# Kernel tuning notes

Measured on AMD Instinct MI355X. Metric: run time of the kernel, lower is better.

Reference implementation:

```python
import jax, jax.numpy as jnp
import numpy as np

V = [642, 2562, 10242]
NGT = 8000
NSAMP = 4000
CHAM_W = [3000.0, 3000.0, 3000.0]
LAP_C = [0.2, 1.0, 1.0]
CHAM_OPP = 0.55
W_LAP, W_MOVE, W_EDGE, W_NORM = 1500.0, 50.0, 359.0, 0.5


def _normalize(x, axis=-1):
    n = jnp.linalg.norm(x, axis=axis, keepdims=True)
    return x / jnp.maximum(n, 1e-12)


def _mse(a, b):
    return jnp.mean((a - b) ** 2)


def _sample_points(verts, faces, n, key):
    # uniform face pick + uniform barycentric (sqrt trick), matches sample_point_cloud
    kf, kb = jax.random.split(key)
    fidx = jax.random.randint(kf, (n,), 0, faces.shape[0])
    tri = verts[faces[fidx]]  # [n,3,3]
    uv = jax.random.uniform(kb, (n, 2), dtype=verts.dtype)
    r1 = jnp.sqrt(uv[:, 0]); r2 = uv[:, 1]
    w = jnp.stack([1.0 - r1, r1 * (1.0 - r2), r1 * r2], axis=1)  # [n,3]
    return jnp.einsum('nk,nkd->nd', w, tri)


def _chamfer(gt, pred):
    # squared pairwise distances [B,Ng,Np]
    d = (jnp.sum(gt ** 2, -1)[:, :, None] + jnp.sum(pred ** 2, -1)[:, None, :]
         - 2.0 * jnp.einsum('bnd,bmd->bnm', gt, pred))
    dist1 = jnp.min(d, 2); idx1 = jnp.argmin(d, 2)  # gt -> nearest pred
    dist2 = jnp.min(d, 1); idx2 = jnp.argmin(d, 1)  # pred -> nearest gt
    return dist1, dist2, idx1, idx2


def _laplace_coord(x, lap):
    # x [B,n,3], lap [n,10]: 8 neighbor idx (-1 invalid), self idx, count
    idx = lap[:, :8]
    mask = idx < 0
    safe = jnp.where(mask, 0, idx)
    v = x[:, safe]  # [B,n,8,3]
    v = jnp.where(mask[None, :, :, None], 0.0, v)
    cnt = lap[:, -1].astype(x.dtype)
    return x - v.sum(2) / cnt[None, :, None]


def _block(gt, gtn, pred, pred_bef, lap, edges, faces, key, cham_w, lap_c, block_idx):
    samp = _sample_points(pred[0], faces, NSAMP, key)[None]
    sample_pred = jnp.concatenate([pred, samp], 1)
    d1, d2, _i1, i2 = _chamfer(gt, sample_pred)
    chamfer = cham_w * (jnp.mean(d1) + CHAM_OPP * jnp.mean(d2))
    e = _normalize(pred[:, edges[:, 0]] - pred[:, edges[:, 1]], 2)
    nn = jnp.take_along_axis(gtn, i2[..., None], axis=1)  # nearest gt normal per pred pt
    nrm = _normalize(nn[:, edges[:, 0]], 2)
    normal = jnp.mean(jnp.abs(jnp.sum(e * nrm, 2)))
    edge = _mse(pred[:, edges[:, 0]], pred[:, edges[:, 1]]) * 3.0
    lap_l = lap_c * _mse(_laplace_coord(pred_bef, lap), _laplace_coord(pred, lap)) * 3.0
    move = lap_c * _mse(pred_bef, pred) * 3.0 if block_idx > 0 else 0.0
    return chamfer, normal, edge, lap_l, move


def setup_inputs() -> dict:
    key = jax.random.key(0)
    ks = jax.random.split(key, 8)
    inp = {}
    inp['gt_points'] = jax.random.normal(ks[0], (1, NGT, 3), jnp.float32)
    inp['gt_normals'] = _normalize(jax.random.normal(ks[1], (1, NGT, 3), jnp.float32), 2)
    for i, v in enumerate(V):
        kp, kb, ke, kf, kl = jax.random.split(ks[2 + i], 5)
        pc = jax.random.normal(kp, (1, v, 3), jnp.float32)
        inp[f'pred_coord_{i}'] = pc
        inp[f'pred_before_{i}'] = pc + 0.1 * jax.random.normal(kb, (1, v, 3), jnp.float32)
        inp[f'edges_{i}'] = jax.random.randint(ke, (3 * v, 2), 0, v, dtype=jnp.int32)
        inp[f'faces_{i}'] = jax.random.randint(kf, (2 * v, 3), 0, v, dtype=jnp.int32)
        nbr = jax.random.randint(kl, (v, 8), 0, v, dtype=jnp.int32)
        valid = (nbr % 7) != 0
        valid = valid.at[:, 0].set(True)  # count >= 1
        cnt = valid.sum(1).astype(jnp.int32)
        nbr_m = jnp.where(valid, nbr, -1)
        self_idx = jnp.arange(v, dtype=jnp.int32)[:, None]
        inp[f'lap_idx_{i}'] = jnp.concatenate([nbr_m, self_idx, cnt[:, None]], 1)
    return inp


def reference(gt_points, gt_normals,
              pred_coord_0, pred_before_0, edges_0, faces_0, lap_idx_0,
              pred_coord_1, pred_before_1, edges_1, faces_1, lap_idx_1,
              pred_coord_2, pred_before_2, edges_2, faces_2, lap_idx_2):
    skey = jax.random.key(42)
    preds = [pred_coord_0, pred_coord_1, pred_coord_2]
    befs = [pred_before_0, pred_before_1, pred_before_2]
    edges = [edges_0, edges_1, edges_2]
    faces = [faces_0, faces_1, faces_2]
    laps = [lap_idx_0, lap_idx_1, lap_idx_2]
    ch = nl = el = ll = ml = 0.0
    for i in range(3):
        c, n, e, l, m = _block(gt_points, gt_normals, preds[i], befs[i], laps[i],
                               edges[i], faces[i], jax.random.fold_in(skey, i),
                               CHAM_W[i], LAP_C[i], i)
        ch += c; nl += n; el += e; ll += l; ml += m
    loss = ch + W_LAP * ll + W_MOVE * ml + W_EDGE * el + W_NORM * nl
    return loss
```

## Files before the change

kernel.cpp:

```cpp
#include <hip/hip_runtime.h>
#include <stdint.h>

#define NGT 8000
#define NSAMP 4000
#define QT 4
#define QB 1024
#define CH 384

struct Params {
  const float* gt;
  const float* gtn;
  const float* pred[3];
  const float* bef[3];
  const int*   edges[3];
  const int*   faces[3];
  const int*   lap[3];
  float* S[3];
  unsigned int* mb1[3];
  unsigned long long* mb2a[3];
  unsigned int* mb2b[3];
  float* acc;
  unsigned int* counter;
  unsigned int* init_base;
  int init_words;
  int v[3], M[3], E[3], F[3];
  int z1, z2;
};

__device__ __forceinline__ unsigned int ford(float f){
  unsigned int b = __float_as_uint(f);
  return b ^ ((b >> 31) ? 0xFFFFFFFFu : 0x80000000u);
}
__device__ __forceinline__ float funord(unsigned int u){
  unsigned int b = u ^ ((u >> 31) ? 0x80000000u : 0xFFFFFFFFu);
  return __uint_as_float(b);
}

__device__ __forceinline__ uint32_t rotl32(uint32_t x, int d){ return (x<<d)|(x>>(32-d)); }

__device__ __forceinline__ void tf2x32(uint32_t k0, uint32_t k1, uint32_t c0, uint32_t c1,
                                       uint32_t& o0, uint32_t& o1){
  uint32_t ks2 = k0 ^ k1 ^ 0x1BD11BDAu;
  uint32_t x0 = c0 + k0, x1 = c1 + k1;
  x0+=x1; x1=rotl32(x1,13); x1^=x0;
  x0+=x1; x1=rotl32(x1,15); x1^=x0;
  x0+=x1; x1=rotl32(x1,26); x1^=x0;
  x0+=x1; x1=rotl32(x1, 6); x1^=x0;
  x0+=k1; x1+=ks2+1u;
  x0+=x1; x1=rotl32(x1,17); x1^=x0;
  x0+=x1; x1=rotl32(x1,29); x1^=x0;
  x0+=x1; x1=rotl32(x1,16); x1^=x0;
  x0+=x1; x1=rotl32(x1,24); x1^=x0;
  x0+=ks2; x1+=k0+2u;
  x0+=x1; x1=rotl32(x1,13); x1^=x0;
  x0+=x1; x1=rotl32(x1,15); x1^=x0;
  x0+=x1; x1=rotl32(x1,26); x1^=x0;
  x0+=x1; x1=rotl32(x1, 6); x1^=x0;
  x0+=k0; x1+=k1+3u;
  x0+=x1; x1=rotl32(x1,17); x1^=x0;
  x0+=x1; x1=rotl32(x1,29); x1^=x0;
  x0+=x1; x1=rotl32(x1,16); x1^=x0;
  x0+=x1; x1=rotl32(x1,24); x1^=x0;
  x0+=k1; x1+=ks2+4u;
  x0+=x1; x1=rotl32(x1,13); x1^=x0;
  x0+=x1; x1=rotl32(x1,15); x1^=x0;
  x0+=x1; x1=rotl32(x1,26); x1^=x0;
  x0+=x1; x1=rotl32(x1, 6); x1^=x0;
  x0+=ks2; x1+=k0+5u;
  o0=x0; o1=x1;
}

__device__ __forceinline__ uint32_t rbits(uint32_t k0, uint32_t k1, uint32_t idx, uint32_t total){
  uint32_t half = total>>1, o0, o1;
  if (idx < half){ tf2x32(k0,k1, idx, idx+half, o0, o1); return o0; }
  tf2x32(k0,k1, idx-half, idx, o0, o1); return o1;
}

__global__ __launch_bounds__(256) void prep_kernel(Params p){
  if (blockIdx.z == 0){
    if (blockIdx.y != 0) return;
    int wdi = blockIdx.x*256 + threadIdx.x;
    if (wdi < p.init_words)
      p.init_base[wdi] = (wdi < 64) ? 0u : 0xFFFFFFFFu;
    return;
  }
  int i = blockIdx.y;
  int s = blockIdx.x*256 + threadIdx.x;
  if (s >= NSAMP) return;
  uint32_t bk0, bk1; tf2x32(0u, 42u, 0u, (uint32_t)i, bk0, bk1);
  uint32_t a0,b0,a1,b1;
  tf2x32(bk0,bk1, 0u,2u, a0,b0);
  tf2x32(bk0,bk1, 1u,3u, a1,b1);
  uint32_t fb = rbits(a0,a1,(uint32_t)s, NSAMP);
  uint32_t fidx = fb % (uint32_t)p.F[i];
  uint32_t u0b = rbits(b0,b1, 2u*(uint32_t)s,    2u*NSAMP);
  uint32_t u1b = rbits(b0,b1, 2u*(uint32_t)s+1u, 2u*NSAMP);
  float u0 = __uint_as_float((u0b>>9)|0x3F800000u) - 1.0f;
  float u1 = __uint_as_float((u1b>>9)|0x3F800000u) - 1.0f;
  float r1 = sqrtf(u0);
  float w0 = 1.0f - r1, w1 = r1*(1.0f-u1), w2 = r1*u1;
  const int* f = p.faces[i] + 3*(int)fidx;
  const float* pr = p.pred[i];
  int va=f[0], vb=f[1], vc=f[2];
  float* dst = p.S[i] + 3*s;
  dst[0] = w0*pr[3*va+0] + w1*pr[3*vb+0] + w2*pr[3*vc+0];
  dst[1] = w0*pr[3*va+1] + w1*pr[3*vb+1] + w2*pr[3*vc+1];
  dst[2] = w0*pr[3*va+2] + w1*pr[3*vb+2] + w2*pr[3*vc+2];
}

__global__ __launch_bounds__(256) void chamfer_kernel(Params p){
  int i = blockIdx.y;
  int v = p.v[i];
  int M = p.M[i];
  int z = blockIdx.z;
  __shared__ float4 tile[CH];
  int t = threadIdx.x;
  int qbase = blockIdx.x*QB;

  if (z < p.z1){
    if (qbase >= NGT) return;
    int c0 = z*CH;
    if (c0 >= M) return;
    int c1 = min(M, c0+CH);
    int lim = c1 - c0;

    for (int jj=t; jj<lim; jj+=256){
      int j = c0 + jj;
      const float* src = (j < v) ? (p.pred[i] + 3*j) : (p.S[i] + 3*(j-v));
      float x=src[0], y=src[1], zz=src[2];
      tile[jj] = make_float4(x,y,zz, x*x+y*y+zz*zz);
    }

    float qx[QT], qy[QT], qz[QT], qs[QT], best[QT];
    #pragma unroll
    for (int k=0;k<QT;k++){
      int q = qbase + t + k*256;
      float x=0.f,y=0.f,zz=0.f;
      if (q < NGT){ x=p.gt[3*q]; y=p.gt[3*q+1]; zz=p.gt[3*q+2]; }
      qs[k]=x*x+y*y+zz*zz; qx[k]=-2.f*x; qy[k]=-2.f*y; qz[k]=-2.f*zz;
      best[k]=3.4e38f;
    }
    __syncthreads();

    int lim2 = lim & ~1;
    #pragma unroll 2
    for (int k=0;k<lim2;k+=2){
      float4 g0 = tile[k];
      float4 g1 = tile[k+1];
      #pragma unroll
      for (int q=0;q<QT;q++){
        float d0 = fmaf(g0.x,qx[q], fmaf(g0.y,qy[q], fmaf(g0.z,qz[q], g0.w)));
        float d1 = fmaf(g1.x,qx[q], fmaf(g1.y,qy[q], fmaf(g1.z,qz[q], g1.w)));
        best[q] = fminf(fminf(best[q], d0), d1);
      }
    }
    if (lim2 < lim){
      float4 g0 = tile[lim2];
      #pragma unroll
      for (int q=0;q<QT;q++){
        float d0 = fmaf(g0.x,qx[q], fmaf(g0.y,qy[q], fmaf(g0.z,qz[q], g0.w)));
        best[q] = fminf(best[q], d0);
      }
    }
    #pragma unroll
    for (int k=0;k<QT;k++){
      int q = qbase + t + k*256;
      if (q < NGT) atomicMin(&p.mb1[i][q], ford(best[k]+qs[k]));
    }
  } else if (z < p.z1 + p.z2){
    if (qbase >= v) return;
    int c0 = (z - p.z1)*CH;
    int c1 = min(NGT, c0+CH);
    int lim = c1 - c0;

    for (int jj=t; jj<lim; jj+=256){
      int j = c0 + jj;
      float x=p.gt[3*j], y=p.gt[3*j+1], zz=p.gt[3*j+2];
      tile[jj] = make_float4(x,y,zz, x*x+y*y+zz*zz);
    }

    float qx[QT], qy[QT], qz[QT], qs[QT], best[QT];
    int bidx[QT];
    #pragma unroll
    for (int k=0;k<QT;k++){
      int q = qbase + t + k*256;
      float x=0.f,y=0.f,zz=0.f;
      if (q < v){
        const float* src = p.pred[i] + 3*q;
        x=src[0]; y=src[1]; zz=src[2];
      }
      qs[k]=x*x+y*y+zz*zz; qx[k]=-2.f*x; qy[k]=-2.f*y; qz[k]=-2.f*zz;
      best[k]=3.4e38f; bidx[k]=0;
    }
    __syncthreads();

    #pragma unroll 4
    for (int k=0;k<lim;k++){
      float4 g = tile[k];
      #pragma unroll
      for (int q=0;q<QT;q++){
        float d = fmaf(g.x,qx[q], fmaf(g.y,qy[q], fmaf(g.z,qz[q], g.w)));
        if (d < best[q]){ best[q]=d; bidx[q]=c0+k; }
      }
    }
    #pragma unroll
    for (int k=0;k<QT;k++){
      int q = qbase + t + k*256;
      if (q < v){
        unsigned long long pk = ((unsigned long long)ford(best[k]+qs[k])<<32) | (unsigned int)bidx[k];
        atomicMin(&p.mb2a[i][q], pk);
      }
    }
  } else {
    if (qbase >= NSAMP) return;
    int c0 = (z - p.z1 - p.z2)*CH;
    int c1 = min(NGT, c0+CH);
    int lim = c1 - c0;

    for (int jj=t; jj<lim; jj+=256){
      int j = c0 + jj;
      float x=p.gt[3*j], y=p.gt[3*j+1], zz=p.gt[3*j+2];
      tile[jj] = make_float4(x,y,zz, x*x+y*y+zz*zz);
    }

    float qx[QT], qy[QT], qz[QT], qs[QT], best[QT];
    #pragma unroll
    for (int k=0;k<QT;k++){
      int q = qbase + t + k*256;
      float x=0.f,y=0.f,zz=0.f;
      if (q < NSAMP){
        const float* src = p.S[i] + 3*q;
        x=src[0]; y=src[1]; zz=src[2];
      }
      qs[k]=x*x+y*y+zz*zz; qx[k]=-2.f*x; qy[k]=-2.f*y; qz[k]=-2.f*zz;
      best[k]=3.4e38f;
    }
    __syncthreads();

    int lim2 = lim & ~1;
    #pragma unroll 2
    for (int k=0;k<lim2;k+=2){
      float4 g0 = tile[k];
      float4 g1 = tile[k+1];
      #pragma unroll
      for (int q=0;q<QT;q++){
        float d0 = fmaf(g0.x,qx[q], fmaf(g0.y,qy[q], fmaf(g0.z,qz[q], g0.w)));
        float d1 = fmaf(g1.x,qx[q], fmaf(g1.y,qy[q], fmaf(g1.z,qz[q], g1.w)));
        best[q] = fminf(fminf(best[q], d0), d1);
      }
    }
    if (lim2 < lim){
      float4 g0 = tile[lim2];
      #pragma unroll
      for (int q=0;q<QT;q++){
        float d0 = fmaf(g0.x,qx[q], fmaf(g0.y,qy[q], fmaf(g0.z,qz[q], g0.w)));
        best[q] = fminf(best[q], d0);
      }
    }
    #pragma unroll
    for (int k=0;k<QT;k++){
      int q = qbase + t + k*256;
      if (q < NSAMP) atomicMin(&p.mb2b[i][q], ford(best[k]+qs[k]));
    }
  }
}

__global__ __launch_bounds__(256) void finish_kernel(Params p, float* out){
  __shared__ float red[256];
  int i = blockIdx.y;
  int z = blockIdx.z;
  int tid = threadIdx.x;
  int gidx = blockIdx.x*256 + tid;

  if (z == 0){
    int M = p.M[i], v = p.v[i];
    float val = 0.f;
    if (gidx < M){
      if (gidx < v) val = funord((unsigned int)(p.mb2a[i][gidx]>>32));
      else          val = funord(p.mb2b[i][gidx-v]);
    }
    red[tid] = val; __syncthreads();
    for (int s=128;s>0;s>>=1){ if (tid<s) red[tid]+=red[tid+s]; __syncthreads(); }
    if (tid==0 && red[0]!=0.f) atomicAdd(&p.acc[8*i+1], red[0]);
  } else if (z == 1){
    float val = 0.f;
    if (gidx < NGT) val = funord(p.mb1[i][gidx]);
    red[tid] = val; __syncthreads();
    for (int s=128;s>0;s>>=1){ if (tid<s) red[tid]+=red[tid+s]; __syncthreads(); }
    if (tid==0 && red[0]!=0.f) atomicAdd(&p.acc[8*i+0], red[0]);
  } else if (z == 2){
    int E = p.E[i];
    float sq = 0.f, ad = 0.f;
    if (gidx < E){
      int e0 = p.edges[i][2*gidx], e1 = p.edges[i][2*gidx+1];
      const float* pr = p.pred[i];
      float dx = pr[3*e0+0]-pr[3*e1+0];
      float dy = pr[3*e0+1]-pr[3*e1+1];
      float dz = pr[3*e0+2]-pr[3*e1+2];
      sq = dx*dx+dy*dy+dz*dz;
      float inv = 1.0f / fmaxf(sqrtf(sq), 1e-12f);
      int g = (int)(unsigned int)p.mb2a[i][e0];
      float nx = p.gtn[3*g+0], ny = p.gtn[3*g+1], nz = p.gtn[3*g+2];
      float invg = 1.0f / fmaxf(sqrtf(nx*nx+ny*ny+nz*nz), 1e-12f);
      ad = fabsf((dx*nx+dy*ny+dz*nz)*inv*invg);
    }
    red[tid] = ad; __syncthreads();
    for (int s=128;s>0;s>>=1){ if (tid<s) red[tid]+=red[tid+s]; __syncthreads(); }
    if (tid==0 && red[0]!=0.f) atomicAdd(&p.acc[8*i+2], red[0]);
    __syncthreads();
    red[tid] = sq; __syncthreads();
    for (int s=128;s>0;s>>=1){ if (tid<s) red[tid]+=red[tid+s]; __syncthreads(); }
    if (tid==0 && red[0]!=0.f) atomicAdd(&p.acc[8*i+3], red[0]);
  } else {
    int v = p.v[i];
    float lsq = 0.f, msq = 0.f;
    if (gidx < v){
      const int* L = p.lap[i] + 10*gidx;
      const float* B = p.bef[i];
      const float* R = p.pred[i];
      float cnt = (float)L[9];
      float sb0=0,sb1=0,sb2=0, sp0=0,sp1=0,sp2=0;
      #pragma unroll
      for (int k=0;k<8;k++){
        int id = L[k];
        if (id >= 0){
          sb0 += B[3*id+0]; sb1 += B[3*id+1]; sb2 += B[3*id+2];
          sp0 += R[3*id+0]; sp1 += R[3*id+1]; sp2 += R[3*id+2];
        }
      }
      float lb0 = B[3*gidx+0] - sb0/cnt, lb1 = B[3*gidx+1] - sb1/cnt, lb2 = B[3*gidx+2] - sb2/cnt;
      float lp0 = R[3*gidx+0] - sp0/cnt, lp1 = R[3*gidx+1] - sp1/cnt, lp2 = R[3*gidx+2] - sp2/cnt;
      float d0=lb0-lp0, d1=lb1-lp1, d2=lb2-lp2;
      lsq = d0*d0+d1*d1+d2*d2;
      float m0=B[3*gidx+0]-R[3*gidx+0], m1=B[3*gidx+1]-R[3*gidx+1], m2=B[3*gidx+2]-R[3*gidx+2];
      msq = m0*m0+m1*m1+m2*m2;
    }
    red[tid] = lsq; __syncthreads();
    for (int s=128;s>0;s>>=1){ if (tid<s) red[tid]+=red[tid+s]; __syncthreads(); }
    if (tid==0 && red[0]!=0.f) atomicAdd(&p.acc[8*i+4], red[0]);
    __syncthreads();
    red[tid] = msq; __syncthreads();
    for (int s=128;s>0;s>>=1){ if (tid<s) red[tid]+=red[tid+s]; __syncthreads(); }
    if (tid==0 && red[0]!=0.f) atomicAdd(&p.acc[8*i+5], red[0]);
  }

  __syncthreads();
  if (tid == 0){
    __threadfence();
    unsigned int total = gridDim.x*gridDim.y*gridDim.z;
    unsigned int old = atomicAdd(p.counter, 1u);
    if (old == total-1){
      __threadfence();
      const float CHAMW[3] = {3000.0f, 3000.0f, 3000.0f};
      const float LAPC[3]  = {0.2f, 1.0f, 1.0f};
      float loss = 0.0f;
      for (int m=0;m<3;m++){
        float a0 = __hip_atomic_load(&p.acc[8*m+0], __ATOMIC_RELAXED, __HIP_MEMORY_SCOPE_AGENT);
        float a1 = __hip_atomic_load(&p.acc[8*m+1], __ATOMIC_RELAXED, __HIP_MEMORY_SCOPE_AGENT);
        float a2 = __hip_atomic_load(&p.acc[8*m+2], __ATOMIC_RELAXED, __HIP_MEMORY_SCOPE_AGENT);
        float a3 = __hip_atomic_load(&p.acc[8*m+3], __ATOMIC_RELAXED, __HIP_MEMORY_SCOPE_AGENT);
        float a4 = __hip_atomic_load(&p.acc[8*m+4], __ATOMIC_RELAXED, __HIP_MEMORY_SCOPE_AGENT);
        float a5 = __hip_atomic_load(&p.acc[8*m+5], __ATOMIC_RELAXED, __HIP_MEMORY_SCOPE_AGENT);
        float ch = CHAMW[m]*(a0/(float)NGT + 0.55f*a1/(float)p.M[m]);
        float nl = a2/(float)p.E[m];
        float el = a3/(float)p.E[m];
        float ll = LAPC[m]*a4/(float)p.v[m];
        float ml = (m>0) ? LAPC[m]*a5/(float)p.v[m] : 0.0f;
        loss += ch + 1500.0f*ll + 50.0f*ml + 359.0f*el + 0.5f*nl;
      }
      out[0] = loss;
    }
  }
}

extern "C" void kernel_launch(void* const* d_in, const int* in_sizes, int n_in,
                              void* d_out, int out_size, void* d_ws, size_t ws_size,
                              hipStream_t stream) {
  Params p;
  p.gt  = (const float*)d_in[0];
  p.gtn = (const float*)d_in[1];
  for (int i=0;i<3;i++){
    p.pred[i]  = (const float*)d_in[2+5*i];
    p.bef[i]   = (const float*)d_in[3+5*i];
    p.edges[i] = (const int*)  d_in[4+5*i];
    p.faces[i] = (const int*)  d_in[5+5*i];
    p.lap[i]   = (const int*)  d_in[6+5*i];
    p.v[i] = in_sizes[2+5*i]/3;
    p.E[i] = in_sizes[4+5*i]/2;
    p.F[i] = in_sizes[5+5*i]/3;
    p.M[i] = p.v[i] + NSAMP;
  }
  unsigned int* base = (unsigned int*)d_ws;
  p.acc = (float*)base;
  p.counter = base + 32;
  p.init_base = base;
  unsigned int* w = base + 64;
  for (int i=0;i<3;i++){ p.mb1[i]  = w; w += NGT; }
  for (int i=0;i<3;i++){ p.mb2a[i] = (unsigned long long*)w; w += 2*p.v[i]; }
  for (int i=0;i<3;i++){ p.mb2b[i] = w; w += NSAMP; }
  p.init_words = (int)(w - base);
  for (int i=0;i<3;i++){ p.S[i] = (float*)w; w += NSAMP*3; }

  int maxM = p.M[0], maxE = p.E[0], maxV = p.v[0];
  for (int i=1;i<3;i++){
    if (p.M[i]>maxM) maxM=p.M[i];
    if (p.E[i]>maxE) maxE=p.E[i];
    if (p.v[i]>maxV) maxV=p.v[i];
  }
  int Z1 = (maxM + CH-1)/CH;
  int Z2 = (NGT + CH-1)/CH;
  p.z1 = Z1; p.z2 = Z2;
  int gx1 = (NGT + QB-1)/QB;
  int gx2 = (maxV + QB-1)/QB;
  int gx3 = (NSAMP + QB-1)/QB;
  int gxB = gx1;
  if (gx2 > gxB) gxB = gx2;
  if (gx3 > gxB) gxB = gx3;

  int gxA = (p.init_words + 255)/256;
  int gxC = (maxE + 255)/256;

  prep_kernel   <<<dim3(gxA, 3, 2),        256, 0, stream>>>(p);
  chamfer_kernel<<<dim3(gxB, 3, Z1+2*Z2),  256, 0, stream>>>(p);
  finish_kernel <<<dim3(gxC, 3, 4),        256, 0, stream>>>(p, (float*)d_out);
}
```

Before: 183.6 us.

## Compact grids into per-segment 1D launches and raise per-thread query count

Replaces the padded 3D grids of all three kernels with flat 1D grids whose block ranges are computed per (role, mesh) segment. This removes the many empty blocks that exited early because every mesh was sized to the largest one. The chamfer kernel now keeps 8 queries per thread over smaller 256-point tiles, and the min/argmin scans are unrolled by 8 and 4 to get more reuse of each loaded tile point. The costs are higher register pressure and fewer queries split across blocks, which can lower occupancy and parallelism on the small meshes.

```diff
diff --git a/kernel.cpp b/kernel.cpp
--- a/kernel.cpp
+++ b/kernel.cpp
@@ -3,9 +3,9 @@
 
 #define NGT 8000
 #define NSAMP 4000
-#define QT 4
-#define QB 1024
-#define CH 384
+#define QT 8
+#define QB 2048
+#define CH 256
 
 struct Params {
   const float* gt;
@@ -23,8 +23,11 @@
   unsigned int* counter;
   unsigned int* init_base;
   int init_words;
+  int prep_init_blocks;
   int v[3], M[3], E[3], F[3];
-  int z1, z2;
+  int cseg[10];
+  int cnc[9];
+  int fseg[13];
 };
 
 __device__ __forceinline__ unsigned int ford(float f){
@@ -77,24 +80,26 @@
 }
 
 __global__ __launch_bounds__(256) void prep_kernel(Params p){
-  if (blockIdx.z == 0){
-    if (blockIdx.y != 0) return;
-    int wdi = blockIdx.x*256 + threadIdx.x;
+  int b = blockIdx.x;
+  int t = threadIdx.x;
+  if (b < p.prep_init_blocks){
+    int wdi = b*256 + t;
     if (wdi < p.init_words)
       p.init_base[wdi] = (wdi < 64) ? 0u : 0xFFFFFFFFu;
     return;
   }
-  int i = blockIdx.y;
-  int s = blockIdx.x*256 + threadIdx.x;
+  int rem = b - p.prep_init_blocks;
+  int i = rem >> 4;
+  int s = ((rem & 15) << 8) + t;
   if (s >= NSAMP) return;
   uint32_t bk0, bk1; tf2x32(0u, 42u, 0u, (uint32_t)i, bk0, bk1);
-  uint32_t a0,b0,a1,b1;
-  tf2x32(bk0,bk1, 0u,2u, a0,b0);
-  tf2x32(bk0,bk1, 1u,3u, a1,b1);
-  uint32_t fb = rbits(a0,a1,(uint32_t)s, NSAMP);
+  uint32_t ka0,kb0,ka1,kb1;
+  tf2x32(bk0,bk1, 0u,2u, ka0,kb0);
+  tf2x32(bk0,bk1, 1u,3u, ka1,kb1);
+  uint32_t fb = rbits(ka0,ka1,(uint32_t)s, NSAMP);
   uint32_t fidx = fb % (uint32_t)p.F[i];
-  uint32_t u0b = rbits(b0,b1, 2u*(uint32_t)s,    2u*NSAMP);
-  uint32_t u1b = rbits(b0,b1, 2u*(uint32_t)s+1u, 2u*NSAMP);
+  uint32_t u0b = rbits(kb0,kb1, 2u*(uint32_t)s,    2u*NSAMP);
+  uint32_t u1b = rbits(kb0,kb1, 2u*(uint32_t)s+1u, 2u*NSAMP);
   float u0 = __uint_as_float((u0b>>9)|0x3F800000u) - 1.0f;
   float u1 = __uint_as_float((u1b>>9)|0x3F800000u) - 1.0f;
   float r1 = sqrtf(u0);
@@ -108,101 +113,136 @@
   dst[2] = w0*pr[3*va+2] + w1*pr[3*vb+2] + w2*pr[3*vc+2];
 }
 
+__device__ __forceinline__ float dist_e(const float4 g, float qx, float qy, float qz){
+  return fmaf(g.x,qx, fmaf(g.y,qy, fmaf(g.z,qz, g.w)));
+}
+
+__device__ __forceinline__ void scan_min(const float4* __restrict__ tile, int lim,
+    const float* qx, const float* qy, const float* qz, float* best)
+{
+  int k = 0;
+  int lim8 = lim & ~7;
+  for (; k < lim8; k += 8){
+    float4 g0=tile[k+0],g1=tile[k+1],g2=tile[k+2],g3=tile[k+3];
+    float4 g4=tile[k+4],g5=tile[k+5],g6=tile[k+6],g7=tile[k+7];
+    #pragma unroll
+    for (int q=0;q<QT;q++){
+      float d0=dist_e(g0,qx[q],qy[q],qz[q]);
+      float d1=dist_e(g1,qx[q],qy[q],qz[q]);
+      float d2=dist_e(g2,qx[q],qy[q],qz[q]);
+      float d3=dist_e(g3,qx[q],qy[q],qz[q]);
+      float d4=dist_e(g4,qx[q],qy[q],qz[q]);
+      float d5=dist_e(g5,qx[q],qy[q],qz[q]);
+      float d6=dist_e(g6,qx[q],qy[q],qz[q]);
+      float d7=dist_e(g7,qx[q],qy[q],qz[q]);
+      float m = fminf(fminf(best[q], d0), d1);
+      m = fminf(fminf(m, d2), d3);
+      m = fminf(fminf(m, d4), d5);
+      m = fminf(fminf(m, d6), d7);
+      best[q] = m;
+    }
+  }
+  for (; k < lim; k++){
+    float4 g = tile[k];
+    #pragma unroll
+    for (int q=0;q<QT;q++)
+      best[q] = fminf(best[q], dist_e(g,qx[q],qy[q],qz[q]));
+  }
+}
+
+__device__ __forceinline__ void scan_argmin(const float4* __restrict__ tile, int lim, int c0,
+    const float* qx, const float* qy, const float* qz, float* best, int* bidx)
+{
+  int k = 0;
+  int lim4 = lim & ~3;
+  for (; k < lim4; k += 4){
+    float4 g0=tile[k+0],g1=tile[k+1],g2=tile[k+2],g3=tile[k+3];
+    #pragma unroll
+    for (int q=0;q<QT;q++){
+      float d0=dist_e(g0,qx[q],qy[q],qz[q]);
+      float d1=dist_e(g1,qx[q],qy[q],qz[q]);
+      float d2=dist_e(g2,qx[q],qy[q],qz[q]);
+      float d3=dist_e(g3,qx[q],qy[q],qz[q]);
+      if (d0 < best[q]){ best[q]=d0; bidx[q]=c0+k+0; }
+      if (d1 < best[q]){ best[q]=d1; bidx[q]=c0+k+1; }
+      if (d2 < best[q]){ best[q]=d2; bidx[q]=c0+k+2; }
+      if (d3 < best[q]){ best[q]=d3; bidx[q]=c0+k+3; }
+    }
+  }
+  for (; k < lim; k++){
+    float4 g = tile[k];
+    #pragma unroll
+    for (int q=0;q<QT;q++){
+      float d = dist_e(g,qx[q],qy[q],qz[q]);
+      if (d < best[q]){ best[q]=d; bidx[q]=c0+k; }
+    }
+  }
+}
+
 __global__ __launch_bounds__(256) void chamfer_kernel(Params p){
-  int i = blockIdx.y;
+  __shared__ float4 tile[CH];
+  int b = blockIdx.x;
+  int seg = 0;
+  #pragma unroll
+  for (int s=1;s<9;s++) seg += (b >= p.cseg[s]) ? 1 : 0;
+  int rem  = b - p.cseg[seg];
+  int nc   = p.cnc[seg];
+  int cq   = rem / nc;
+  int cc   = rem - cq*nc;
+  int role = seg / 3;
+  int i    = seg - role*3;
+  int t = threadIdx.x;
+  int qbase = cq*QB;
+  int c0 = cc*CH;
   int v = p.v[i];
-  int M = p.M[i];
-  int z = blockIdx.z;
-  __shared__ float4 tile[CH];
-  int t = threadIdx.x;
-  int qbase = blockIdx.x*QB;
-
-  if (z < p.z1){
-    if (qbase >= NGT) return;
-    int c0 = z*CH;
-    if (c0 >= M) return;
-    int c1 = min(M, c0+CH);
-    int lim = c1 - c0;
-
-    for (int jj=t; jj<lim; jj+=256){
-      int j = c0 + jj;
+
+  if (role == 0){
+    int M = p.M[i];
+    int lim = min(M - c0, CH);
+    if (t < lim){
+      int j = c0 + t;
       const float* src = (j < v) ? (p.pred[i] + 3*j) : (p.S[i] + 3*(j-v));
-      float x=src[0], y=src[1], zz=src[2];
-      tile[jj] = make_float4(x,y,zz, x*x+y*y+zz*zz);
-    }
-
-    float qx[QT], qy[QT], qz[QT], qs[QT], best[QT];
-    #pragma unroll
-    for (int k=0;k<QT;k++){
-      int q = qbase + t + k*256;
-      float x=0.f,y=0.f,zz=0.f;
-      if (q < NGT){ x=p.gt[3*q]; y=p.gt[3*q+1]; zz=p.gt[3*q+2]; }
-      qs[k]=x*x+y*y+zz*zz; qx[k]=-2.f*x; qy[k]=-2.f*y; qz[k]=-2.f*zz;
+      float x=src[0], y=src[1], z=src[2];
+      tile[t] = make_float4(x,y,z, x*x+y*y+z*z);
+    }
+    float qx[QT],qy[QT],qz[QT],qs[QT],best[QT];
+    #pragma unroll
+    for (int k=0;k<QT;k++){
+      int q = qbase + t + k*256;
+      float x=0.f,y=0.f,z=0.f;
+      if (q < NGT){ x=p.gt[3*q]; y=p.gt[3*q+1]; z=p.gt[3*q+2]; }
+      qs[k]=x*x+y*y+z*z; qx[k]=-2.f*x; qy[k]=-2.f*y; qz[k]=-2.f*z;
       best[k]=3.4e38f;
     }
     __syncthreads();
-
-    int lim2 = lim & ~1;
-    #pragma unroll 2
-    for (int k=0;k<lim2;k+=2){
-      float4 g0 = tile[k];
-      float4 g1 = tile[k+1];
-      #pragma unroll
-      for (int q=0;q<QT;q++){
-        float d0 = fmaf(g0.x,qx[q], fmaf(g0.y,qy[q], fmaf(g0.z,qz[q], g0.w)));
-        float d1 = fmaf(g1.x,qx[q], fmaf(g1.y,qy[q], fmaf(g1.z,qz[q], g1.w)));
-        best[q] = fminf(fminf(best[q], d0), d1);
-      }
-    }
-    if (lim2 < lim){
-      float4 g0 = tile[lim2];
-      #pragma unroll
-      for (int q=0;q<QT;q++){
-        float d0 = fmaf(g0.x,qx[q], fmaf(g0.y,qy[q], fmaf(g0.z,qz[q], g0.w)));
-        best[q] = fminf(best[q], d0);
-      }
-    }
+    scan_min(tile, lim, qx,qy,qz,best);
     #pragma unroll
     for (int k=0;k<QT;k++){
       int q = qbase + t + k*256;
       if (q < NGT) atomicMin(&p.mb1[i][q], ford(best[k]+qs[k]));
     }
-  } else if (z < p.z1 + p.z2){
-    if (qbase >= v) return;
-    int c0 = (z - p.z1)*CH;
-    int c1 = min(NGT, c0+CH);
-    int lim = c1 - c0;
-
-    for (int jj=t; jj<lim; jj+=256){
-      int j = c0 + jj;
-      float x=p.gt[3*j], y=p.gt[3*j+1], zz=p.gt[3*j+2];
-      tile[jj] = make_float4(x,y,zz, x*x+y*y+zz*zz);
-    }
-
-    float qx[QT], qy[QT], qz[QT], qs[QT], best[QT];
+  } else if (role == 1){
+    int lim = min(NGT - c0, CH);
+    if (t < lim){
+      int j = c0 + t;
+      float x=p.gt[3*j], y=p.gt[3*j+1], z=p.gt[3*j+2];
+      tile[t] = make_float4(x,y,z, x*x+y*y+z*z);
+    }
+    float qx[QT],qy[QT],qz[QT],qs[QT],best[QT];
     int bidx[QT];
     #pragma unroll
     for (int k=0;k<QT;k++){
       int q = qbase + t + k*256;
-      float x=0.f,y=0.f,zz=0.f;
+      float x=0.f,y=0.f,z=0.f;
       if (q < v){
         const float* src = p.pred[i] + 3*q;
-        x=src[0]; y=src[1]; zz=src[2];
+        x=src[0]; y=src[1]; z=src[2];
       }
-      qs[k]=x*x+y*y+zz*zz; qx[k]=-2.f*x; qy[k]=-2.f*y; qz[k]=-2.f*zz;
+      qs[k]=x*x+y*y+z*z; qx[k]=-2.f*x; qy[k]=-2.f*y; qz[k]=-2.f*z;
       best[k]=3.4e38f; bidx[k]=0;
     }
     __syncthreads();
-
-    #pragma unroll 4
-    for (int k=0;k<lim;k++){
-      float4 g = tile[k];
-      #pragma unroll
-      for (int q=0;q<QT;q++){
-        float d = fmaf(g.x,qx[q], fmaf(g.y,qy[q], fmaf(g.z,qz[q], g.w)));
-        if (d < best[q]){ best[q]=d; bidx[q]=c0+k; }
-      }
-    }
+    scan_argmin(tile, lim, c0, qx,qy,qz,best,bidx);
     #pragma unroll
     for (int k=0;k<QT;k++){
       int q = qbase + t + k*256;
@@ -212,51 +252,26 @@
       }
     }
   } else {
-    if (qbase >= NSAMP) return;
-    int c0 = (z - p.z1 - p.z2)*CH;
-    int c1 = min(NGT, c0+CH);
-    int lim = c1 - c0;
-
-    for (int jj=t; jj<lim; jj+=256){
-      int j = c0 + jj;
-      float x=p.gt[3*j], y=p.gt[3*j+1], zz=p.gt[3*j+2];
-      tile[jj] = make_float4(x,y,zz, x*x+y*y+zz*zz);
-    }
-
-    float qx[QT], qy[QT], qz[QT], qs[QT], best[QT];
-    #pragma unroll
-    for (int k=0;k<QT;k++){
-      int q = qbase + t + k*256;
-      float x=0.f,y=0.f,zz=0.f;
+    int lim = min(NGT - c0, CH);
+    if (t < lim){
+      int j = c0 + t;
+      float x=p.gt[3*j], y=p.gt[3*j+1], z=p.gt[3*j+2];
+      tile[t] = make_float4(x,y,z, x*x+y*y+z*z);
+    }
+    float qx[QT],qy[QT],qz[QT],qs[QT],best[QT];
+    #pragma unroll
+    for (int k=0;k<QT;k++){
+      int q = qbase + t + k*256;
+      float x=0.f,y=0.f,z=0.f;
       if (q < NSAMP){
         const float* src = p.S[i] + 3*q;
-        x=src[0]; y=src[1]; zz=src[2];
+        x=src[0]; y=src[1]; z=src[2];
       }
-      qs[k]=x*x+y*y+zz*zz; qx[k]=-2.f*x; qy[k]=-2.f*y; qz[k]=-2.f*zz;
+      qs[k]=x*x+y*y+z*z; qx[k]=-2.f*x; qy[k]=-2.f*y; qz[k]=-2.f*z;
       best[k]=3.4e38f;
     }
     __syncthreads();
-
-    int lim2 = lim & ~1;
-    #pragma unroll 2
-    for (int k=0;k<lim2;k+=2){
-      float4 g0 = tile[k];
-      float4 g1 = tile[k+1];
-      #pragma unroll
-      for (int q=0;q<QT;q++){
-        float d0 = fmaf(g0.x,qx[q], fmaf(g0.y,qy[q], fmaf(g0.z,qz[q], g0.w)));
-        float d1 = fmaf(g1.x,qx[q], fmaf(g1.y,qy[q], fmaf(g1.z,qz[q], g1.w)));
-        best[q] = fminf(fminf(best[q], d0), d1);
-      }
-    }
-    if (lim2 < lim){
-      float4 g0 = tile[lim2];
-      #pragma unroll
-      for (int q=0;q<QT;q++){
-        float d0 = fmaf(g0.x,qx[q], fmaf(g0.y,qy[q], fmaf(g0.z,qz[q], g0.w)));
-        best[q] = fminf(best[q], d0);
-      }
-    }
+    scan_min(tile, lim, qx,qy,qz,best);
     #pragma unroll
     for (int k=0;k<QT;k++){
       int q = qbase + t + k*256;
@@ -267,10 +282,15 @@
 
 __global__ __launch_bounds__(256) void finish_kernel(Params p, float* out){
   __shared__ float red[256];
-  int i = blockIdx.y;
-  int z = blockIdx.z;
+  int b = blockIdx.x;
+  int seg = 0;
+  #pragma unroll
+  for (int s=1;s<12;s++) seg += (b >= p.fseg[s]) ? 1 : 0;
+  int rem = b - p.fseg[seg];
+  int z = seg / 3;
+  int i = seg - 3*z;
   int tid = threadIdx.x;
-  int gidx = blockIdx.x*256 + tid;
+  int gidx = rem*256 + tid;
 
   if (z == 0){
     int M = p.M[i], v = p.v[i];
@@ -347,7 +367,7 @@
   __syncthreads();
   if (tid == 0){
     __threadfence();
-    unsigned int total = gridDim.x*gridDim.y*gridDim.z;
+    unsigned int total = gridDim.x;
     unsigned int old = atomicAdd(p.counter, 1u);
     if (old == total-1){
       __threadfence();
@@ -401,26 +421,29 @@
   p.init_words = (int)(w - base);
   for (int i=0;i<3;i++){ p.S[i] = (float*)w; w += NSAMP*3; }
 
-  int maxM = p.M[0], maxE = p.E[0], maxV = p.v[0];
-  for (int i=1;i<3;i++){
-    if (p.M[i]>maxM) maxM=p.M[i];
-    if (p.E[i]>maxE) maxE=p.E[i];
-    if (p.v[i]>maxV) maxV=p.v[i];
-  }
-  int Z1 = (maxM + CH-1)/CH;
-  int Z2 = (NGT + CH-1)/CH;
-  p.z1 = Z1; p.z2 = Z2;
-  int gx1 = (NGT + QB-1)/QB;
-  int gx2 = (maxV + QB-1)/QB;
-  int gx3 = (NSAMP + QB-1)/QB;
-  int gxB = gx1;
-  if (gx2 > gxB) gxB = gx2;
-  if (gx3 > gxB) gxB = gx3;
-
-  int gxA = (p.init_words + 255)/256;
-  int gxC = (maxE + 255)/256;
-
-  prep_kernel   <<<dim3(gxA, 3, 2),        256, 0, stream>>>(p);
-  chamfer_kernel<<<dim3(gxB, 3, Z1+2*Z2),  256, 0, stream>>>(p);
-  finish_kernel <<<dim3(gxC, 3, 4),        256, 0, stream>>>(p, (float*)d_out);
-}
+  int cnq[9];
+  for (int i=0;i<3;i++){
+    cnq[0+i] = (NGT + QB-1)/QB;           p.cnc[0+i] = (p.M[i] + CH-1)/CH;
+    cnq[3+i] = (p.v[i] + QB-1)/QB;        p.cnc[3+i] = (NGT + CH-1)/CH;
+    cnq[6+i] = (NSAMP + QB-1)/QB;         p.cnc[6+i] = (NGT + CH-1)/CH;
+  }
+  p.cseg[0] = 0;
+  for (int s=0;s<9;s++) p.cseg[s+1] = p.cseg[s] + cnq[s]*p.cnc[s];
+
+  int fn[12];
+  for (int i=0;i<3;i++){
+    fn[0+i] = (p.M[i] + 255)/256;
+    fn[3+i] = (NGT + 255)/256;
+    fn[6+i] = (p.E[i] + 255)/256;
+    fn[9+i] = (p.v[i] + 255)/256;
+  }
+  p.fseg[0] = 0;
+  for (int s=0;s<12;s++) p.fseg[s+1] = p.fseg[s] + fn[s];
+
+  int initB = (p.init_words + 255)/256;
+  p.prep_init_blocks = initB;
+
+  prep_kernel   <<<dim3(initB + 3*16), 256, 0, stream>>>(p);
+  chamfer_kernel<<<dim3(p.cseg[9]),    256, 0, stream>>>(p);
+  finish_kernel <<<dim3(p.fseg[12]),   256, 0, stream>>>(p, (float*)d_out);
+}
```

New measurement: 154.1 us. -16.1%, faster.
